# Kernel tuning notes

Hardware: AMD Instinct MI355X
Metric: run time of the kernel (lower is better)

## Reference

```python
import jax, jax.numpy as jnp
import numpy as np

N = 1048576        # number of time samples (rays)
V = 32             # num_videos
D = 32             # embedding_dim
F = 6              # num_frequencies
K = 2 * F + 1      # basis size: [1, sin(2^j*pi*t), cos(2^j*pi*t)]


def setup_inputs() -> dict:
    key = jax.random.key(0)
    k1, k2, k3 = jax.random.split(key, 3)
    times = jax.random.uniform(k1, (N, 1), dtype=jnp.float32)
    video_ids = jax.random.randint(k2, (N, 1), 0, V, dtype=jnp.int32)
    weights = jax.random.normal(k3, (V, D, K), dtype=jnp.float32)
    return {"times": times, "video_ids": video_ids, "weights": weights}


def _fourier_basis(t):
    # t: [N] -> [N, K] with basis [1, sin(2^j pi t), cos(2^j pi t)] j=0..F-1
    freqs = (2.0 ** jnp.arange(F, dtype=t.dtype)) * jnp.pi  # [F]
    ang = t[:, None] * freqs                                # [N, F]
    return jnp.concatenate(
        [jnp.ones_like(t)[:, None], jnp.sin(ang), jnp.cos(ang)], axis=-1
    )


def reference(times, video_ids, weights):
    shp = times.shape
    t = times.reshape(-1)                       # [N]
    vid = video_ids.reshape(-1).astype(jnp.int32)  # [N]
    basis = _fourier_basis(t)                   # [N, K]
    w = weights[vid]                            # gather: [N, D, K]
    emb = jnp.einsum('ndk,nk->nd', w, basis)    # [N, D]
    return emb.reshape((*shp[:-1], -1))
```

## Files before the change

kernel.cpp:

```cpp
#include <hip/hip_runtime.h>
#include <hip/hip_fp16.h>

#define NRAYS 1048576
#define NV 32
#define ND 32
#define NF 6
#define NK 13

typedef _Float16 h2 __attribute__((ext_vector_type(2)));
typedef float f4 __attribute__((ext_vector_type(4)));

__device__ __forceinline__ float fdot2acc(h2 a, h2 b, float c) {
#if __has_builtin(__builtin_amdgcn_fdot2)
    return __builtin_amdgcn_fdot2(a, b, c, false);
#else
    return c + (float)a.x * (float)b.x + (float)a.y * (float)b.y;
#endif
}

__device__ __forceinline__ h2 pack2(float a, float b) {
#if __has_builtin(__builtin_amdgcn_cvt_pkrtz)
    return __builtin_bit_cast(h2, __builtin_amdgcn_cvt_pkrtz(a, b));
#else
    h2 r; r.x = (_Float16)a; r.y = (_Float16)b; return r;
#endif
}

__device__ __forceinline__ float hwsin(float rev) {
#if __has_builtin(__builtin_amdgcn_sinf)
    return __builtin_amdgcn_sinf(rev);
#else
    return __sinf(6.28318530717958647692f * rev);
#endif
}
__device__ __forceinline__ float hwcos(float rev) {
#if __has_builtin(__builtin_amdgcn_cosf)
    return __builtin_amdgcn_cosf(rev);
#else
    return __cosf(6.28318530717958647692f * rev);
#endif
}

__global__ __launch_bounds__(256, 5) void VideoEmbedding_kernel(
    const float* __restrict__ times,
    const int* __restrict__ vids,
    const float* __restrict__ weights,
    float* __restrict__ out)
{
    __shared__ _Float16 wl[NV * 7 * ND * 2];

    const int tid = threadIdx.x;

    for (int j = tid; j < NV * ND; j += 256) {
        int v = j >> 5, d = j & 31;
        wl[v * 448 + 6 * 64 + d * 2 + 1] = (_Float16)0.f;
    }
    for (int j = tid; j < NV * ND * NK; j += 256) {
        int v = j / (ND * NK);
        int r = j - v * (ND * NK);
        int d = r / NK;
        int k = r - d * NK;
        wl[v * 448 + (k >> 1) * 64 + d * 2 + (k & 1)] = (_Float16)weights[j];
    }
    __syncthreads();

    const int q = tid & 7;
    int ray = ((blockIdx.x * 256) + tid) >> 3;
    const int nslots = (gridDim.x * 256) >> 3;

    float t = 0.f;
    int vid = 0;
    if (ray < NRAYS) {
        t = times[ray];
        vid = vids[ray];
    }

    while (ray < NRAYS) {
        const int nray = ray + nslots;
        float tn = 0.f;
        int vidn = 0;
        if (nray < NRAYS) {
            tn = times[nray];
            vidn = vids[nray];
        }

        float sv[NF], cv[NF];
        float rev = 0.5f * t;
#pragma unroll
        for (int j = 0; j < NF; ++j) {
            sv[j] = hwsin(rev);
            cv[j] = hwcos(rev);
            rev += rev;
        }

        h2 bp[7];
        bp[0] = pack2(1.0f, sv[0]);
        bp[1] = pack2(sv[1], sv[2]);
        bp[2] = pack2(sv[3], sv[4]);
        bp[3] = pack2(sv[5], cv[0]);
        bp[4] = pack2(cv[1], cv[2]);
        bp[5] = pack2(cv[3], cv[4]);
        bp[6] = pack2(cv[5], 0.0f);

        const unsigned base = (unsigned)vid * 448u + (unsigned)q * 8u;
        uint4 w[7];
#pragma unroll
        for (int i = 0; i < 7; ++i)
            w[i] = *reinterpret_cast<const uint4*>(&wl[base + i * 64]);

        float a0 = 0.f, a1 = 0.f, a2 = 0.f, a3 = 0.f;
#pragma unroll
        for (int i = 0; i < 7; ++i) {
            h2 w0 = __builtin_bit_cast(h2, w[i].x);
            h2 w1 = __builtin_bit_cast(h2, w[i].y);
            h2 w2 = __builtin_bit_cast(h2, w[i].z);
            h2 w3 = __builtin_bit_cast(h2, w[i].w);
            a0 = fdot2acc(w0, bp[i], a0);
            a1 = fdot2acc(w1, bp[i], a1);
            a2 = fdot2acc(w2, bp[i], a2);
            a3 = fdot2acc(w3, bp[i], a3);
        }

        f4 res;
        res.x = a0; res.y = a1; res.z = a2; res.w = a3;
        __builtin_nontemporal_store(res, reinterpret_cast<f4*>(out) + (size_t)ray * 8 + q);

        ray = nray;
        t = tn;
        vid = vidn;
    }
}

extern "C" void kernel_launch(void* const* d_in, const int* in_sizes, int n_in,
                              void* d_out, int out_size, void* d_ws, size_t ws_size,
                              hipStream_t stream) {
    const float* times = (const float*)d_in[0];
    const int* vids = (const int*)d_in[1];
    const float* weights = (const float*)d_in[2];
    float* out = (float*)d_out;

    dim3 grid(1280), block(256);
    hipLaunchKernelGGL(VideoEmbedding_kernel, grid, block, 0, stream,
                       times, vids, weights, out);
}
```

Before: 39.23 us.

## Pre-pack fp16 weights in a separate kernel and deepen input prefetch

A small pre-kernel converts the fp32 weights into the packed fp16 pair layout in workspace. Each main-kernel block then copies it into LDS with seven vectorized 16-byte loads, replacing the per-block scalar conversion loop with its integer divisions. The time/vid prefetch now runs two iterations ahead instead of one. The output store changes from nontemporal to a regular store. The extra launch adds overhead, and the changed store may alter cache behavior.

Measured after the change: 37.59 us. 1.04x faster.

```diff
diff --git a/kernel.cpp b/kernel.cpp
--- a/kernel.cpp
+++ b/kernel.cpp
@@ -41,51 +41,58 @@
 #endif
 }
 
+__global__ void pack_weights_kernel(const float* __restrict__ weights,
+                                    unsigned* __restrict__ wpack)
+{
+    int j = blockIdx.x * 256 + threadIdx.x;
+    if (j >= NV * 7 * ND) return;
+    int v = j >> 8;
+    v = j / 224;
+    int r = j - v * 224;
+    int i = r >> 5;
+    int d = r & 31;
+    float w0 = weights[v * (ND * NK) + d * NK + 2 * i];
+    float w1 = (2 * i + 1 < NK) ? weights[v * (ND * NK) + d * NK + 2 * i + 1] : 0.f;
+    h2 p = pack2(w0, w1);
+    wpack[v * 224 + i * 32 + d] = __builtin_bit_cast(unsigned, p);
+}
+
 __global__ __launch_bounds__(256, 5) void VideoEmbedding_kernel(
     const float* __restrict__ times,
     const int* __restrict__ vids,
-    const float* __restrict__ weights,
+    const unsigned* __restrict__ wpack,
     float* __restrict__ out)
 {
     __shared__ _Float16 wl[NV * 7 * ND * 2];
 
     const int tid = threadIdx.x;
 
-    for (int j = tid; j < NV * ND; j += 256) {
-        int v = j >> 5, d = j & 31;
-        wl[v * 448 + 6 * 64 + d * 2 + 1] = (_Float16)0.f;
-    }
-    for (int j = tid; j < NV * ND * NK; j += 256) {
-        int v = j / (ND * NK);
-        int r = j - v * (ND * NK);
-        int d = r / NK;
-        int k = r - d * NK;
-        wl[v * 448 + (k >> 1) * 64 + d * 2 + (k & 1)] = (_Float16)weights[j];
+    {
+        const uint4* src = reinterpret_cast<const uint4*>(wpack);
+        uint4* dst = reinterpret_cast<uint4*>(wl);
+#pragma unroll
+        for (int j = 0; j < 7; ++j)
+            dst[tid + j * 256] = src[tid + j * 256];
     }
     __syncthreads();
 
     const int q = tid & 7;
+    const int nslots = (gridDim.x * 256) >> 3;
     int ray = ((blockIdx.x * 256) + tid) >> 3;
-    const int nslots = (gridDim.x * 256) >> 3;
 
-    float t = 0.f;
-    int vid = 0;
-    if (ray < NRAYS) {
-        t = times[ray];
-        vid = vids[ray];
-    }
+    int rA = ray < NRAYS ? ray : 0;
+    int rB = ray + nslots < NRAYS ? ray + nslots : 0;
+    float tA = times[rA], tB = times[rB];
+    int vA = vids[rA], vB = vids[rB];
 
     while (ray < NRAYS) {
-        const int nray = ray + nslots;
-        float tn = 0.f;
-        int vidn = 0;
-        if (nray < NRAYS) {
-            tn = times[nray];
-            vidn = vids[nray];
-        }
+        const int ray2 = ray + 2 * nslots;
+        const int rC = ray2 < NRAYS ? ray2 : 0;
+        const float tC = times[rC];
+        const int vC = vids[rC];
 
         float sv[NF], cv[NF];
-        float rev = 0.5f * t;
+        float rev = 0.5f * tA;
 #pragma unroll
         for (int j = 0; j < NF; ++j) {
             sv[j] = hwsin(rev);
@@ -102,7 +109,7 @@
         bp[5] = pack2(cv[3], cv[4]);
         bp[6] = pack2(cv[5], 0.0f);
 
-        const unsigned base = (unsigned)vid * 448u + (unsigned)q * 8u;
+        const unsigned base = (unsigned)vA * 448u + (unsigned)q * 8u;
         uint4 w[7];
 #pragma unroll
         for (int i = 0; i < 7; ++i)
@@ -111,23 +118,19 @@
         float a0 = 0.f, a1 = 0.f, a2 = 0.f, a3 = 0.f;
 #pragma unroll
         for (int i = 0; i < 7; ++i) {
-            h2 w0 = __builtin_bit_cast(h2, w[i].x);
-            h2 w1 = __builtin_bit_cast(h2, w[i].y);
-            h2 w2 = __builtin_bit_cast(h2, w[i].z);
-            h2 w3 = __builtin_bit_cast(h2, w[i].w);
-            a0 = fdot2acc(w0, bp[i], a0);
-            a1 = fdot2acc(w1, bp[i], a1);
-            a2 = fdot2acc(w2, bp[i], a2);
-            a3 = fdot2acc(w3, bp[i], a3);
+            a0 = fdot2acc(__builtin_bit_cast(h2, w[i].x), bp[i], a0);
+            a1 = fdot2acc(__builtin_bit_cast(h2, w[i].y), bp[i], a1);
+            a2 = fdot2acc(__builtin_bit_cast(h2, w[i].z), bp[i], a2);
+            a3 = fdot2acc(__builtin_bit_cast(h2, w[i].w), bp[i], a3);
         }
 
         f4 res;
         res.x = a0; res.y = a1; res.z = a2; res.w = a3;
-        __builtin_nontemporal_store(res, reinterpret_cast<f4*>(out) + (size_t)ray * 8 + q);
+        reinterpret_cast<f4*>(out)[(size_t)ray * 8 + q] = res;
 
-        ray = nray;
-        t = tn;
-        vid = vidn;
+        ray += nslots;
+        tA = tB; vA = vB;
+        tB = tC; vB = vC;
     }
 }
 
@@ -138,8 +141,10 @@
     const int* vids = (const int*)d_in[1];
     const float* weights = (const float*)d_in[2];
     float* out = (float*)d_out;
+    unsigned* wpack = (unsigned*)d_ws;
 
-    dim3 grid(1280), block(256);
-    hipLaunchKernelGGL(VideoEmbedding_kernel, grid, block, 0, stream,
-                       times, vids, weights, out);
+    hipLaunchKernelGGL(pack_weights_kernel, dim3(28), dim3(256), 0, stream,
+                       weights, wpack);
+    hipLaunchKernelGGL(VideoEmbedding_kernel, dim3(1280), dim3(256), 0, stream,
+                       times, vids, wpack, out);
 }
```

## Bucket rays by video id before computing embeddings per video segment

Applied to the files above, without the earlier changes.

Adds a scatter pass that counts rays per video id in a block histogram and appends (time, ray index) records into fixed-capacity per-video segments. The main kernel then gives each block a single video, so it stages only that video's weights in shared memory instead of converting the whole weight table in every block. The sine/cosine chain now uses double-angle recurrences in place of repeated hardware sin/cos calls. This costs an extra memset, a second launch and a scatter write/read round trip, the output writes become scattered, and any segment beyond the fixed capacity silently drops rays.

Result: slower. 53.64 us (+36.7%).

```diff
diff --git a/kernel.cpp b/kernel.cpp
--- a/kernel.cpp
+++ b/kernel.cpp
@@ -6,6 +6,7 @@
 #define ND 32
 #define NF 6
 #define NK 13
+#define SEG_CAP 36864
 
 typedef _Float16 h2 __attribute__((ext_vector_type(2)));
 typedef float f4 __attribute__((ext_vector_type(4)));
@@ -41,56 +42,84 @@
 #endif
 }
 
-__global__ __launch_bounds__(256, 5) void VideoEmbedding_kernel(
+__global__ __launch_bounds__(256) void scatter_kernel(
     const float* __restrict__ times,
     const int* __restrict__ vids,
+    int* __restrict__ cursors,
+    uint2* __restrict__ recs)
+{
+    __shared__ int hist[NV], hbase[NV], hist2[NV];
+    const int tid = threadIdx.x;
+    if (tid < NV) { hist[tid] = 0; hist2[tid] = 0; }
+    __syncthreads();
+
+    const int base = blockIdx.x * 1024;
+    float t[4]; int v[4], r[4];
+#pragma unroll
+    for (int it = 0; it < 4; ++it) {
+        r[it] = base + it * 256 + tid;
+        t[it] = times[r[it]];
+        v[it] = vids[r[it]];
+        atomicAdd(&hist[v[it]], 1);
+    }
+    __syncthreads();
+    if (tid < NV) hbase[tid] = atomicAdd(&cursors[tid], hist[tid]);
+    __syncthreads();
+#pragma unroll
+    for (int it = 0; it < 4; ++it) {
+        int rank = atomicAdd(&hist2[v[it]], 1);
+        int slot = hbase[v[it]] + rank;
+        if (slot < SEG_CAP) {
+            uint2 rec;
+            rec.x = __builtin_bit_cast(unsigned, t[it]);
+            rec.y = (unsigned)r[it];
+            recs[v[it] * SEG_CAP + slot] = rec;
+        }
+    }
+}
+
+__global__ __launch_bounds__(256, 6) void VideoEmbedding_kernel(
     const float* __restrict__ weights,
+    const int* __restrict__ cursors,
+    const uint2* __restrict__ recs,
     float* __restrict__ out)
 {
-    __shared__ _Float16 wl[NV * 7 * ND * 2];
+    __shared__ _Float16 wl[7 * 64];
 
     const int tid = threadIdx.x;
+    const int seg = blockIdx.x / 48;
+    const int c = blockIdx.x % 48;
 
-    for (int j = tid; j < NV * ND; j += 256) {
-        int v = j >> 5, d = j & 31;
-        wl[v * 448 + 6 * 64 + d * 2 + 1] = (_Float16)0.f;
-    }
-    for (int j = tid; j < NV * ND * NK; j += 256) {
-        int v = j / (ND * NK);
-        int r = j - v * (ND * NK);
-        int d = r / NK;
-        int k = r - d * NK;
-        wl[v * 448 + (k >> 1) * 64 + d * 2 + (k & 1)] = (_Float16)weights[j];
+    if (tid < 224) {
+        int i = tid >> 5, d = tid & 31;
+        const float* wp = weights + seg * (ND * NK) + d * NK;
+        float w0 = wp[2 * i];
+        float w1 = (2 * i + 1 < NK) ? wp[2 * i + 1] : 0.f;
+        reinterpret_cast<unsigned*>(wl)[tid] =
+            __builtin_bit_cast(unsigned, pack2(w0, w1));
     }
     __syncthreads();
 
+    const int count = min(cursors[seg], SEG_CAP);
+    const uint2* srec = recs + seg * SEG_CAP;
     const int q = tid & 7;
-    int ray = ((blockIdx.x * 256) + tid) >> 3;
-    const int nslots = (gridDim.x * 256) >> 3;
+    const int g = tid >> 3;
 
-    float t = 0.f;
-    int vid = 0;
-    if (ray < NRAYS) {
-        t = times[ray];
-        vid = vids[ray];
-    }
-
-    while (ray < NRAYS) {
-        const int nray = ray + nslots;
-        float tn = 0.f;
-        int vidn = 0;
-        if (nray < NRAYS) {
-            tn = times[nray];
-            vidn = vids[nray];
-        }
+    for (int r0 = c * 32; r0 < count; r0 += 48 * 32) {
+        const int ridx = r0 + g;
+        const bool valid = ridx < count;
+        const uint2 rec = srec[valid ? ridx : count - 1];
+        const float t = __builtin_bit_cast(float, rec.x);
+        const int ray = (int)rec.y;
 
         float sv[NF], cv[NF];
-        float rev = 0.5f * t;
+        sv[0] = hwsin(0.5f * t);
+        cv[0] = hwcos(0.5f * t);
 #pragma unroll
-        for (int j = 0; j < NF; ++j) {
-            sv[j] = hwsin(rev);
-            cv[j] = hwcos(rev);
-            rev += rev;
+        for (int j = 1; j < NF; ++j) {
+            float sj = sv[j - 1], cj = cv[j - 1];
+            sv[j] = 2.f * sj * cj;
+            cv[j] = fmaf(-2.f * sj, sj, 1.f);
         }
 
         h2 bp[7];
@@ -102,32 +131,21 @@
         bp[5] = pack2(cv[3], cv[4]);
         bp[6] = pack2(cv[5], 0.0f);
 
-        const unsigned base = (unsigned)vid * 448u + (unsigned)q * 8u;
-        uint4 w[7];
-#pragma unroll
-        for (int i = 0; i < 7; ++i)
-            w[i] = *reinterpret_cast<const uint4*>(&wl[base + i * 64]);
-
         float a0 = 0.f, a1 = 0.f, a2 = 0.f, a3 = 0.f;
 #pragma unroll
         for (int i = 0; i < 7; ++i) {
-            h2 w0 = __builtin_bit_cast(h2, w[i].x);
-            h2 w1 = __builtin_bit_cast(h2, w[i].y);
-            h2 w2 = __builtin_bit_cast(h2, w[i].z);
-            h2 w3 = __builtin_bit_cast(h2, w[i].w);
-            a0 = fdot2acc(w0, bp[i], a0);
-            a1 = fdot2acc(w1, bp[i], a1);
-            a2 = fdot2acc(w2, bp[i], a2);
-            a3 = fdot2acc(w3, bp[i], a3);
+            uint4 w = *reinterpret_cast<const uint4*>(&wl[i * 64 + q * 8]);
+            a0 = fdot2acc(__builtin_bit_cast(h2, w.x), bp[i], a0);
+            a1 = fdot2acc(__builtin_bit_cast(h2, w.y), bp[i], a1);
+            a2 = fdot2acc(__builtin_bit_cast(h2, w.z), bp[i], a2);
+            a3 = fdot2acc(__builtin_bit_cast(h2, w.w), bp[i], a3);
         }
 
-        f4 res;
-        res.x = a0; res.y = a1; res.z = a2; res.w = a3;
-        __builtin_nontemporal_store(res, reinterpret_cast<f4*>(out) + (size_t)ray * 8 + q);
-
-        ray = nray;
-        t = tn;
-        vid = vidn;
+        if (valid) {
+            f4 res;
+            res.x = a0; res.y = a1; res.z = a2; res.w = a3;
+            reinterpret_cast<f4*>(out)[(size_t)ray * 8 + q] = res;
+        }
     }
 }
 
@@ -139,7 +157,12 @@
     const float* weights = (const float*)d_in[2];
     float* out = (float*)d_out;
 
-    dim3 grid(1280), block(256);
-    hipLaunchKernelGGL(VideoEmbedding_kernel, grid, block, 0, stream,
-                       times, vids, weights, out);
+    int* cursors = (int*)d_ws;
+    uint2* recs = (uint2*)((char*)d_ws + 4096);
+
+    hipMemsetAsync(d_ws, 0, 128, stream);
+    hipLaunchKernelGGL(scatter_kernel, dim3(1024), dim3(256), 0, stream,
+                       times, vids, cursors, recs);
+    hipLaunchKernelGGL(VideoEmbedding_kernel, dim3(32 * 48), dim3(256), 0, stream,
+                       weights, cursors, recs, out);
 }
```
